# Kernel tuning notes

Hardware: AMD Instinct MI355X
Metric: run time of the kernel (lower is better)

The kernel has to match this reference:

```python
import jax, jax.numpy as jnp
import numpy as np
from jax import lax

B, S, V, E, H = 128, 256, 50000, 300, 512
Hh = H // 2  # per-direction hidden


def _lstm_dir(x, Wih, Whh, bih, bhh):
    # x: [B,S,E] -> hs: [B,S,Hh]; PyTorch gate order i,f,g,o
    b = x.shape[0]
    h0 = jnp.zeros((b, Hh), x.dtype)
    c0 = jnp.zeros((b, Hh), x.dtype)
    bias = bih + bhh

    def step(carry, xt):
        h, c = carry
        g = xt @ Wih.T + h @ Whh.T + bias  # [B,4Hh]
        i, f, gg, o = jnp.split(g, 4, axis=-1)
        c = jax.nn.sigmoid(f) * c + jax.nn.sigmoid(i) * jnp.tanh(gg)
        h = jax.nn.sigmoid(o) * jnp.tanh(c)
        return (h, c), h

    _, hs = lax.scan(step, (h0, c0), jnp.swapaxes(x, 0, 1))
    return jnp.swapaxes(hs, 0, 1)


def _bilstm(x, p):
    fwd = _lstm_dir(x, p['Wih_f'], p['Whh_f'], p['bih_f'], p['bhh_f'])
    bwd = _lstm_dir(jnp.flip(x, 1), p['Wih_b'], p['Whh_b'], p['bih_b'], p['bhh_b'])
    return jnp.concatenate([fwd, jnp.flip(bwd, 1)], axis=-1)  # [B,S,H]


def _masked_mean(h, length_minus1):
    # mean over first (len-1) timesteps, vectorized replacement for per-sample loop
    mask = (jnp.arange(h.shape[1])[None, :] < length_minus1[:, None]).astype(h.dtype)  # [B,S]
    return jnp.einsum('bsh,bs->bh', h, mask) / length_minus1[:, None].astype(h.dtype)


def setup_inputs() -> dict:
    key = jax.random.key(0)
    ks = jax.random.split(key, 20)
    sc = 0.05
    inp = {
        'x1': jax.random.randint(ks[0], (B, S), 0, V, dtype=jnp.int32),
        'x2': jax.random.randint(ks[1], (B, S), 0, V, dtype=jnp.int32),
        'len1': jax.random.randint(ks[2], (B,), 2, S + 1, dtype=jnp.int32),
        'len2': jax.random.randint(ks[3], (B,), 2, S + 1, dtype=jnp.int32),
        'emb': jax.random.normal(ks[4], (V, E), jnp.float32) * sc,
        'Wih_f': jax.random.normal(ks[5], (4 * Hh, E), jnp.float32) * sc,
        'Whh_f': jax.random.normal(ks[6], (4 * Hh, Hh), jnp.float32) * sc,
        'bih_f': jnp.zeros((4 * Hh,), jnp.float32),
        'bhh_f': jnp.zeros((4 * Hh,), jnp.float32),
        'Wih_b': jax.random.normal(ks[7], (4 * Hh, E), jnp.float32) * sc,
        'Whh_b': jax.random.normal(ks[8], (4 * Hh, Hh), jnp.float32) * sc,
        'bih_b': jnp.zeros((4 * Hh,), jnp.float32),
        'bhh_b': jnp.zeros((4 * Hh,), jnp.float32),
        'W1': jax.random.normal(ks[9], (H, H), jnp.float32) * sc,
        'b1': jnp.zeros((H,), jnp.float32),
        'W2': jax.random.normal(ks[10], (H // 2, H), jnp.float32) * sc,
        'b2': jnp.zeros((H // 2,), jnp.float32),
        'Wo': jax.random.normal(ks[11], (1, H // 2), jnp.float32) * sc,
        'bo': jnp.zeros((1,), jnp.float32),
    }
    return inp


def reference(x1, x2, len1, len2, emb, Wih_f, Whh_f, bih_f, bhh_f,
              Wih_b, Whh_b, bih_b, bhh_b, W1, b1, W2, b2, Wo, bo):
    p = dict(Wih_f=Wih_f, Whh_f=Whh_f, bih_f=bih_f, bhh_f=bhh_f,
             Wih_b=Wih_b, Whh_b=Whh_b, bih_b=bih_b, bhh_b=bhh_b)
    e1 = emb[x1]  # [B,S,E]
    e2 = emb[x2]
    h1 = _bilstm(e1, p)  # [B,S,H]
    h2 = _bilstm(e2, p)
    v1 = _masked_mean(h1, len1 - 1)  # [B,H]
    v2 = _masked_mean(h2, len2 - 1)
    vec = jnp.abs(v1 - v2)  # aggr_type == 'sub'
    a1 = jax.nn.relu(vec @ W1.T + b1)
    a2 = jax.nn.relu(a1 @ W2.T + b2)
    logits = (a2 @ Wo.T + bo)[:, 0]  # [B]
    preds = jax.nn.sigmoid(logits)
    return logits, preds
```

## Files before the change

kernel.cpp:

```cpp
#include <hip/hip_runtime.h>
#include <hip/hip_bf16.h>
#include <math.h>

typedef unsigned short u16;
typedef short s16x8 __attribute__((ext_vector_type(8)));
typedef float f32x4v __attribute__((ext_vector_type(4)));
typedef int i32x4 __attribute__((ext_vector_type(4)));
typedef unsigned short u16x4 __attribute__((ext_vector_type(4)));

#define EDIM 300
#define EPAD 320
#define VOCAB 50000

static constexpr size_t SZ_WIH  = (size_t)2 * 1024 * EPAD * 2;
static constexpr size_t SZ_WPK  = (size_t)2 * 1024 * 256;
static constexpr size_t SZ_SW   = (size_t)2 * 1024 * 4;
static constexpr size_t SZ_BIAS = (size_t)2 * 1024 * 4;
static constexpr size_t SZ_HSV  = (size_t)2 * 256 * 256;
static constexpr size_t SZ_CST  = (size_t)2 * 256 * 256 * 4;
static constexpr size_t SZ_VAC  = (size_t)2 * 256 * 256 * 4;
static constexpr size_t SZ_VOUT = (size_t)2 * 128 * 512 * 4;
static constexpr size_t SZ_EMB  = (size_t)VOCAB * EPAD * 2;
static constexpr size_t SZ_PAD  = (size_t)512 * 1024;
static constexpr size_t FIXED_B = SZ_WIH + SZ_WPK + SZ_SW + SZ_BIAS + SZ_HSV + SZ_CST + SZ_VAC + SZ_VOUT + SZ_EMB + SZ_PAD;
static constexpr size_t SZ_STEP = (size_t)2 * 256 * 1024 * 2;


__device__ __forceinline__ float bf2f(u16 u) {
  union { float f; unsigned int i; } v; v.i = ((unsigned int)u) << 16; return v.f;
}
__device__ __forceinline__ u16 f2bf(float f) {
  union { float f; unsigned int i; } v; v.f = f;
  unsigned int r = v.i + 0x7fffu + ((v.i >> 16) & 1u);
  return (u16)(r >> 16);
}
__device__ __forceinline__ void gload_lds16(const void* g, void* l) {
  __builtin_amdgcn_global_load_lds((const __attribute__((address_space(1))) void*)g,
                                   (__attribute__((address_space(3))) void*)l, 16, 0, 0);
}
__device__ __forceinline__ void lds_barrier() {
  asm volatile("s_waitcnt lgkmcnt(0)" ::: "memory");
  __builtin_amdgcn_s_barrier();
}
__device__ __forceinline__ void wave_lds_fence() {
  asm volatile("s_waitcnt lgkmcnt(0)" ::: "memory");
  __builtin_amdgcn_sched_barrier(0);
}

__global__ void prep_kernel(const float* wih_f, const float* bih_f, const float* bhh_f,
                            const float* wih_b, const float* bih_b, const float* bhh_b,
                            u16* wih_bf, float* bias)
{
  int tid = blockIdx.x * blockDim.x + threadIdx.x;
  if (tid < 2 * 1024 * EPAD) {
    int d = tid / (1024 * EPAD); int rr = tid % (1024 * EPAD);
    int p = rr / EPAD; int k = rr % EPAD;
    int w = p >> 7, q = (p >> 4) & 7, ul = p & 15;
    int jlog = (q & 3) * 256 + w * 32 + (q >> 2) * 16 + ul;
    const float* wsrc = d ? wih_b : wih_f;
    wih_bf[tid] = (k < EDIM) ? f2bf(wsrc[(size_t)jlog * EDIM + k]) : (u16)0;
  }
  int t2 = tid - 2 * 1024 * EPAD;
  if (t2 >= 0 && t2 < 2 * 1024) {
    int d = t2 >> 10; int p = t2 & 1023;
    int w = p >> 7, q = (p >> 4) & 7, ul = p & 15;
    int jlog = (q & 3) * 256 + w * 32 + (q >> 2) * 16 + ul;
    bias[t2] = d ? (bih_b[jlog] + bhh_b[jlog]) : (bih_f[jlog] + bhh_f[jlog]);
  }
}

__global__ void embconv_kernel(const float* emb, u16* embbf)
{
  int r = blockIdx.x;
  int k = threadIdx.x;
  embbf[(size_t)r * EPAD + k] = (k < EDIM) ? f2bf(emb[(size_t)r * EDIM + k]) : (u16)0;
}

__global__ void whhq_kernel(const float* whh_f, const float* whh_b, char* wpk, float* sw)
{
  int jp = blockIdx.x;
  int t = threadIdx.x;
  int d = jp >> 10, p = jp & 1023;
  int w = p >> 7, q = (p >> 4) & 7, ul = p & 15;
  int jlog = (q & 3) * 256 + w * 32 + (q >> 2) * 16 + ul;
  const float* src = (d ? whh_b : whh_f) + (size_t)jlog * 256;
  float v[4]; float m = 0.f;
  #pragma unroll
  for (int kk = 0; kk < 4; ++kk) { v[kk] = src[t * 4 + kk]; m = fmaxf(m, fabsf(v[kk])); }
  #pragma unroll
  for (int off = 32; off > 0; off >>= 1) m = fmaxf(m, __shfl_xor(m, off));
  float sunit = m / 127.f;
  if (sunit < 1e-30f) sunit = 1e-30f;
  unsigned int pk = 0;
  #pragma unroll
  for (int kk = 0; kk < 4; ++kk) {
    int qv = (int)rintf(v[kk] / sunit);
    qv = qv > 127 ? 127 : (qv < -127 ? -127 : qv);
    pk |= ((unsigned int)(qv & 255)) << (8 * kk);
  }
  size_t base = ((((size_t)(d * 8 + w) * 8 + q) * 4 + (t >> 4)) * 64
                 + (((t >> 2) & 3) * 16 + ul)) * 16 + (t & 3) * 4;
  *(unsigned int*)&wpk[base] = pk;
  if (t == 0) sw[jp] = sunit / 127.f;
}

__device__ __forceinline__ void gemm_body(
    int bid, const int* __restrict__ x1, const int* __restrict__ x2,
    const u16* __restrict__ embbf, const u16* __restrict__ wih_bf,
    const float* __restrict__ bias, u16* __restrict__ slab,
    int t0, int T, int logT, char* smem)
{
  u16* Bs = (u16*)smem;
  int d  = bid >> (1 + logT);
  int tl = (bid >> 1) & (T - 1);
  int R0 = (bid & 1) * 128;
  int lane = threadIdx.x & 63;
  int w = threadIdx.x >> 6;

  const int* x = (R0 >> 7) ? x2 : x1;
  int t = t0 + tl;
  int tpos = d ? (255 - t) : t;

  int rowR = R0 + w * 16 + (lane & 15);
  int tok = x[(rowR & 127) * 256 + tpos];
  const char* arow = (const char*)embbf + (size_t)tok * 640 + (lane >> 4) * 16;
  s16x8 areg[10];
  #pragma unroll
  for (int kc = 0; kc < 10; ++kc)
    areg[kc] = *(const s16x8*)(arow + kc * 64);

  const char* Bbase = (const char*)(wih_bf + (size_t)d * 1024 * EPAD);
  int ar  = lane >> 3;
  int acb = (lane & 7) * 16;
  int swz = ar << 4;

  #pragma unroll
  for (int i = 0; i < 2; ++i) {
    int lrow = (i * 8 + w) * 8 + ar;
    gload_lds16(Bbase + (size_t)lrow * 640 + (acb ^ swz),
                (char*)Bs + (i * 8 + w) * 1024);
  }
  __syncthreads();

  size_t rowbase = (size_t)(d * T + tl) * 256 + R0;
  int buf = 0;
  int ul = lane & 15;

  for (int nt = 0; nt < 8; ++nt) {
    f32x4v acc[8] = {};
    #pragma unroll
    for (int kt = 0; kt < 5; ++kt) {
      int nkt = kt + 1, nnt = nt;
      if (nkt == 5) { nkt = 0; nnt = nt + 1; }
      if (nnt < 8) {
        #pragma unroll
        for (int i = 0; i < 2; ++i) {
          int lrow = (i * 8 + w) * 8 + ar;
          gload_lds16(Bbase + (size_t)(nnt * 128 + lrow) * 640 + nkt * 128 + (acb ^ swz),
                      (char*)Bs + (buf ^ 1) * 16384 + (i * 8 + w) * 1024);
        }
      }
      #pragma unroll
      for (int kc2 = 0; kc2 < 2; ++kc2) {
        int cb = kc2 * 64 + (lane >> 4) * 16;
        #pragma unroll
        for (int nf = 0; nf < 8; ++nf) {
          int rr = nf * 16 + (lane & 15);
          s16x8 b = *(const s16x8*)((const char*)Bs + buf * 16384 + rr * 128 + (cb ^ ((rr & 7) << 4)));
          acc[nf] = __builtin_amdgcn_mfma_f32_16x16x32_bf16(areg[kt * 2 + kc2], b, acc[nf], 0, 0, 0);
        }
      }
      __syncthreads();
      buf ^= 1;
    }
    float bv[8];
    #pragma unroll
    for (int nf = 0; nf < 8; ++nf)
      bv[nf] = bias[d * 1024 + nt * 128 + nf * 16 + ul];
    #pragma unroll
    for (int uh = 0; uh < 2; ++uh)
      #pragma unroll
      for (int i = 0; i < 4; ++i) {
        int row = w * 16 + (lane >> 4) * 4 + i;
        u16x4 v;
        #pragma unroll
        for (int g = 0; g < 4; ++g)
          v[g] = f2bf(acc[uh * 4 + g][i] + bv[uh * 4 + g]);
        *(u16x4*)(slab + (rowbase + row) * 1024 + nt * 128 + uh * 64 + ul * 4) = v;
      }
  }
}

__device__ __forceinline__ void lstm_body(
    int bid, const u16* __restrict__ slab, const i32x4* __restrict__ wpk,
    const float* __restrict__ sw, char* hsave,
    float* cstate, float* vaccst, float* vout,
    const int* __restrict__ len1, const int* __restrict__ len2,
    int t0, int T, char* smem)
{
  char* h = smem;
  int* gst = (int*)(smem + 1152);

  const int d = bid >> 7, bt = bid & 127;
  const int tid = threadIdx.x;
  const int lane = tid & 63, w = tid >> 6;
  const int cl = lane & 15;
  const int cr  = lane >> 5;
  const int cuh = (lane >> 4) & 1;
  const int cu  = w * 32 + cuh * 16 + cl;

  i32x4 bfr[8][4];
  #pragma unroll
  for (int q = 0; q < 8; ++q)
    #pragma unroll
    for (int kc = 0; kc < 4; ++kc)
      bfr[q][kc] = wpk[(((size_t)(d * 8 + w) * 8 + q) * 4 + kc) * 64 + lane];
  float swl4[4];
  #pragma unroll
  for (int g = 0; g < 4; ++g)
    swl4[g] = sw[d * 1024 + w * 128 + (cuh * 4 + g) * 16 + cl];

  const int R0 = bt * 2;
  {
    int r = tid >> 8, u = tid & 255;
    h[r * 288 + u] = (t0 > 0) ? hsave[((size_t)d * 256 + R0 + r) * 256 + u] : (char)0;
  }

  const int RR = R0 + cr;
  const int lm = ((RR >> 7) ? len2 : len1)[RR & 127] - 1;
  const size_t sidx = ((size_t)d * 256 + RR) * 256 + cu;
  float c = 0.f, va = 0.f;
  if (t0 > 0) { c = cstate[sidx]; va = vaccst[sidx]; }

  const size_t GSTEP = (size_t)256 * 1024;
  const u16* gcell = slab + ((size_t)d * T * 256 + RR) * 1024 + w * 128 + cuh * 64 + cl * 4;
  u16x4 gv = *(const u16x4*)gcell;
  __syncthreads();

  const bool final_chunk = (t0 + T == 256);
  int par = 0;

  for (int tl = 0; tl < T; ++tl) {
    u16x4 gvn = *(const u16x4*)(gcell + GSTEP * (size_t)(tl + 1));

    i32x4 a[4] = {{0,0,0,0},{0,0,0,0},{0,0,0,0},{0,0,0,0}};
    if (cl < 2) {
      #pragma unroll
      for (int kc = 0; kc < 4; ++kc)
        a[kc] = *(const i32x4*)&h[(par * 2 + cl) * 288 + kc * 64 + (lane >> 4) * 16];
    }
    i32x4 acc[8];
    #pragma unroll
    for (int q = 0; q < 8; ++q) {
      i32x4 z = {0, 0, 0, 0};
      #pragma unroll
      for (int kc = 0; kc < 4; ++kc)
        z = __builtin_amdgcn_mfma_i32_16x16x64_i8(a[kc], bfr[q][kc], z, 0, 0, 0);
      acc[q] = z;
    }

    if (lane < 16) {
      #pragma unroll
      for (int r2 = 0; r2 < 2; ++r2)
        #pragma unroll
        for (int uh2 = 0; uh2 < 2; ++uh2) {
          i32x4 v = { acc[uh2 * 4 + 0][r2], acc[uh2 * 4 + 1][r2],
                      acc[uh2 * 4 + 2][r2], acc[uh2 * 4 + 3][r2] };
          *(i32x4*)&gst[(w * 64 + r2 * 32 + uh2 * 16 + lane) * 4] = v;
        }
    }
    wave_lds_fence();
    i32x4 g4 = *(const i32x4*)&gst[(w * 64 + lane) * 4];

    {
      float s0 = (float)g4[0] * swl4[0] + bf2f(gv[0]);
      float s1 = (float)g4[1] * swl4[1] + bf2f(gv[1]);
      float s2 = (float)g4[2] * swl4[2] + bf2f(gv[2]);
      float s3 = (float)g4[3] * swl4[3] + bf2f(gv[3]);
      float I = __builtin_amdgcn_rcpf(1.f + __expf(-s0));
      float F = __builtin_amdgcn_rcpf(1.f + __expf(-s1));
      float G = 1.f - 2.f * __builtin_amdgcn_rcpf(__expf(2.f * s2) + 1.f);
      float O = __builtin_amdgcn_rcpf(1.f + __expf(-s3));
      float cn = F * c + I * G;
      c = cn;
      float hn = O * (1.f - 2.f * __builtin_amdgcn_rcpf(__expf(2.f * cn) + 1.f));
      int tmap = d ? (255 - (t0 + tl)) : (t0 + tl);
      if (tmap < lm) va += hn;
      h[((par ^ 1) * 2 + cr) * 288 + cu] = (char)(int)rintf(hn * 127.f);
    }
    lds_barrier();
    gv = gvn;
    par ^= 1;
  }

  cstate[sidx] = c;
  vaccst[sidx] = va;
  if (final_chunk) {
    vout[((size_t)(RR >> 7) * 128 + (RR & 127)) * 512 + d * 256 + cu] = va / (float)lm;
  } else {
    int r = tid >> 8, u = tid & 255;
    hsave[((size_t)d * 256 + R0 + r) * 256 + u] = h[(par * 2 + r) * 288 + u];
  }
}

__global__ void __launch_bounds__(512, 2)
fused_kernel(const int* x1, const int* x2, const u16* embbf, const u16* wih_bf,
             const float* bias, const i32x4* wpk, const float* sw,
             char* hsave, float* cstate, float* vaccst, float* vout,
             const int* len1, const int* len2,
             const u16* lstm_slab, u16* gemm_slab,
             int lstm_t0, int gemm_t0, int nL, int T, int logT)
{
  __shared__ __align__(16) char smem[32768];
  if ((int)blockIdx.x < nL) {
    lstm_body(blockIdx.x, lstm_slab, wpk, sw, hsave, cstate, vaccst, vout,
              len1, len2, lstm_t0, T, smem);
  } else if (gemm_t0 >= 0) {
    gemm_body(blockIdx.x - nL, x1, x2, embbf, wih_bf, bias, gemm_slab,
              gemm_t0, T, logT, smem);
  }
}

__global__ void mlp_kernel(const float* v, const float* W1, const float* b1,
                           const float* W2, const float* b2, const float* Wo, const float* bo,
                           float* out)
{
  __shared__ float vec[512];
  __shared__ float a1[512];
  __shared__ float red[4];
  int b = blockIdx.x;
  int tid = threadIdx.x;
  for (int i = tid; i < 512; i += 256)
    vec[i] = fabsf(v[(size_t)b * 512 + i] - v[(size_t)(128 + b) * 512 + i]);
  __syncthreads();
  for (int j = tid; j < 512; j += 256) {
    float s = b1[j];
    const float* wr = W1 + (size_t)j * 512;
    for (int k = 0; k < 512; ++k) s += vec[k] * wr[k];
    a1[j] = fmaxf(s, 0.f);
  }
  __syncthreads();
  float s = b2[tid];
  {
    const float* wr = W2 + (size_t)tid * 512;
    for (int k = 0; k < 512; ++k) s += a1[k] * wr[k];
  }
  float p = fmaxf(s, 0.f) * Wo[tid];
  for (int off = 32; off > 0; off >>= 1) p += __shfl_down(p, off);
  if ((tid & 63) == 0) red[tid >> 6] = p;
  __syncthreads();
  if (tid == 0) {
    float logit = red[0] + red[1] + red[2] + red[3] + bo[0];
    out[b] = logit;
    out[128 + b] = 1.f / (1.f + __expf(-logit));
  }
}

extern "C" void kernel_launch(void* const* d_in, const int* in_sizes, int n_in,
                              void* d_out, int out_size, void* d_ws, size_t ws_size,
                              hipStream_t stream)
{
  const int*   x1    = (const int*)d_in[0];
  const int*   x2    = (const int*)d_in[1];
  const int*   len1  = (const int*)d_in[2];
  const int*   len2  = (const int*)d_in[3];
  const float* emb   = (const float*)d_in[4];
  const float* wih_f = (const float*)d_in[5];
  const float* whh_f = (const float*)d_in[6];
  const float* bih_f = (const float*)d_in[7];
  const float* bhh_f = (const float*)d_in[8];
  const float* wih_b = (const float*)d_in[9];
  const float* whh_b = (const float*)d_in[10];
  const float* bih_b = (const float*)d_in[11];
  const float* bhh_b = (const float*)d_in[12];
  const float* W1    = (const float*)d_in[13];
  const float* b1    = (const float*)d_in[14];
  const float* W2    = (const float*)d_in[15];
  const float* b2    = (const float*)d_in[16];
  const float* Wo    = (const float*)d_in[17];
  const float* bo    = (const float*)d_in[18];

  char* p = (char*)d_ws;
  u16*   wih_bf = (u16*)p;          p += SZ_WIH;
  char*  wpk    = (char*)p;         p += SZ_WPK;
  float* swp    = (float*)p;        p += SZ_SW;
  float* bias   = (float*)p;        p += SZ_BIAS;
  char*  hsave  = (char*)p;         p += SZ_HSV;
  float* cst    = (float*)p;        p += SZ_CST;
  float* vac    = (float*)p;        p += SZ_VAC;
  float* vout   = (float*)p;        p += SZ_VOUT;
  u16*   embbf  = (u16*)p;          p += SZ_EMB;

  int T = 64;
  while (T > 1 && FIXED_B + (size_t)2 * T * SZ_STEP > ws_size) T >>= 1;
  int logT = __builtin_ctz((unsigned)T);
  u16* slab0 = (u16*)p;             p += (size_t)T * SZ_STEP;
  u16* slab1 = (u16*)p;
  u16* slabs[2] = { slab0, slab1 };

  {
    int total = 2 * 1024 * EPAD + 2 * 1024;
    prep_kernel<<<(total + 255) / 256, 256, 0, stream>>>(
        wih_f, bih_f, bhh_f, wih_b, bih_b, bhh_b, wih_bf, bias);
  }
  whhq_kernel<<<2048, 64, 0, stream>>>(whh_f, whh_b, wpk, swp);
  embconv_kernel<<<VOCAB, EPAD, 0, stream>>>(emb, embbf);

  int NCH = 256 / T;
  fused_kernel<<<4 * T, 512, 0, stream>>>(x1, x2, embbf, wih_bf, bias,
                                          (const i32x4*)wpk, swp, hsave, cst, vac, vout,
                                          len1, len2, slabs[0], slabs[0],
                                          -1, 0, 0, T, logT);
  for (int ch = 1; ch < NCH; ++ch) {
    fused_kernel<<<256 + 4 * T, 512, 0, stream>>>(x1, x2, embbf, wih_bf, bias,
                                                  (const i32x4*)wpk, swp, hsave, cst, vac, vout,
                                                  len1, len2, slabs[(ch - 1) & 1], slabs[ch & 1],
                                                  (ch - 1) * T, ch * T, 256, T, logT);
  }
  fused_kernel<<<256, 512, 0, stream>>>(x1, x2, embbf, wih_bf, bias,
                                        (const i32x4*)wpk, swp, hsave, cst, vac, vout,
                                        len1, len2, slabs[(NCH - 1) & 1], slabs[0],
                                        (NCH - 1) * T, -1, 256, T, logT);

  mlp_kernel<<<128, 256, 0, stream>>>(vout, W1, b1, W2, b2, Wo, bo, (float*)d_out);
}
```

Before: 448.4 us.

## Triple-buffer Wih tiles with vmcnt-based barrier and larger time chunk

```diff
diff --git a/kernel.cpp b/kernel.cpp
--- a/kernel.cpp
+++ b/kernel.cpp
@@ -46,6 +46,10 @@
   asm volatile("s_waitcnt lgkmcnt(0)" ::: "memory");
   __builtin_amdgcn_sched_barrier(0);
 }
+__device__ __forceinline__ void tile_barrier_vm2() {
+  asm volatile("s_waitcnt vmcnt(2)" ::: "memory");
+  __builtin_amdgcn_s_barrier();
+}
 
 __global__ void prep_kernel(const float* wih_f, const float* bih_f, const float* bhh_f,
                             const float* wih_b, const float* bih_b, const float* bhh_b,
@@ -134,44 +138,42 @@
   int acb = (lane & 7) * 16;
   int swz = ar << 4;
 
-  #pragma unroll
-  for (int i = 0; i < 2; ++i) {
-    int lrow = (i * 8 + w) * 8 + ar;
-    gload_lds16(Bbase + (size_t)lrow * 640 + (acb ^ swz),
-                (char*)Bs + (i * 8 + w) * 1024);
-  }
-  __syncthreads();
+  #define ISSUE_TILE(nnt, nkt, b3)                                                     \
+    { _Pragma("unroll")                                                                \
+      for (int i = 0; i < 2; ++i) {                                                    \
+        int lrow = (i * 8 + w) * 8 + ar;                                               \
+        gload_lds16(Bbase + (size_t)((nnt) * 128 + lrow) * 640 + (nkt) * 128 + (acb ^ swz), \
+                    (char*)Bs + (b3) * 16384 + (i * 8 + w) * 1024);                    \
+      } }
+
+  ISSUE_TILE(0, 0, 0);
+  ISSUE_TILE(0, 1, 1);
 
   size_t rowbase = (size_t)(d * T + tl) * 256 + R0;
-  int buf = 0;
   int ul = lane & 15;
 
+  #pragma unroll
   for (int nt = 0; nt < 8; ++nt) {
     f32x4v acc[8] = {};
     #pragma unroll
     for (int kt = 0; kt < 5; ++kt) {
-      int nkt = kt + 1, nnt = nt;
-      if (nkt == 5) { nkt = 0; nnt = nt + 1; }
-      if (nnt < 8) {
-        #pragma unroll
-        for (int i = 0; i < 2; ++i) {
-          int lrow = (i * 8 + w) * 8 + ar;
-          gload_lds16(Bbase + (size_t)(nnt * 128 + lrow) * 640 + nkt * 128 + (acb ^ swz),
-                      (char*)Bs + (buf ^ 1) * 16384 + (i * 8 + w) * 1024);
-        }
+      const int g = nt * 5 + kt;
+      tile_barrier_vm2();
+      {
+        const int g2 = g + 2;
+        if (g2 < 40) ISSUE_TILE(g2 / 5, g2 % 5, g2 % 3);
       }
+      const int b3 = g % 3;
       #pragma unroll
       for (int kc2 = 0; kc2 < 2; ++kc2) {
         int cb = kc2 * 64 + (lane >> 4) * 16;
         #pragma unroll
         for (int nf = 0; nf < 8; ++nf) {
           int rr = nf * 16 + (lane & 15);
-          s16x8 b = *(const s16x8*)((const char*)Bs + buf * 16384 + rr * 128 + (cb ^ ((rr & 7) << 4)));
+          s16x8 b = *(const s16x8*)((const char*)Bs + b3 * 16384 + rr * 128 + (cb ^ ((rr & 7) << 4)));
           acc[nf] = __builtin_amdgcn_mfma_f32_16x16x32_bf16(areg[kt * 2 + kc2], b, acc[nf], 0, 0, 0);
         }
       }
-      __syncthreads();
-      buf ^= 1;
     }
     float bv[8];
     #pragma unroll
@@ -184,11 +186,12 @@
         int row = w * 16 + (lane >> 4) * 4 + i;
         u16x4 v;
         #pragma unroll
-        for (int g = 0; g < 4; ++g)
-          v[g] = f2bf(acc[uh * 4 + g][i] + bv[uh * 4 + g]);
+        for (int g2 = 0; g2 < 4; ++g2)
+          v[g2] = f2bf(acc[uh * 4 + g2][i] + bv[uh * 4 + g2]);
         *(u16x4*)(slab + (rowbase + row) * 1024 + nt * 128 + uh * 64 + ul * 4) = v;
       }
   }
+  #undef ISSUE_TILE
 }
 
 __device__ __forceinline__ void lstm_body(
@@ -311,7 +314,7 @@
              const u16* lstm_slab, u16* gemm_slab,
              int lstm_t0, int gemm_t0, int nL, int T, int logT)
 {
-  __shared__ __align__(16) char smem[32768];
+  __shared__ __align__(16) char smem[49152];
   if ((int)blockIdx.x < nL) {
     lstm_body(blockIdx.x, lstm_slab, wpk, sw, hsave, cstate, vaccst, vout,
               len1, len2, lstm_t0, T, smem);
@@ -391,7 +394,7 @@
   float* vout   = (float*)p;        p += SZ_VOUT;
   u16*   embbf  = (u16*)p;          p += SZ_EMB;
 
-  int T = 64;
+  int T = 128;
   while (T > 1 && FIXED_B + (size_t)2 * T * SZ_STEP > ws_size) T >>= 1;
   int logT = __builtin_ctz((unsigned)T);
   u16* slab0 = (u16*)p;             p += (size_t)T * SZ_STEP;
```

Result: no change. 442.9 us (-1.2%).
